# Kernel tuning notes

Measured on AMD Instinct MI355X. Metric: run time of the kernel, lower is better.

## Reference

```python
import jax, jax.numpy as jnp
import numpy as np

N_NODES = 100000
N_EDGES = 1600000
D_FEAT = 64


def setup_inputs() -> dict:
    key = jax.random.key(0)
    k1, k2 = jax.random.split(key)
    x = jax.random.normal(k1, (N_NODES, D_FEAT), dtype=jnp.float32)
    edge_index = jax.random.randint(k2, (2, N_EDGES), 0, N_NODES, dtype=jnp.int64)
    alpha = jnp.ones((), dtype=jnp.float32)
    res_scale = jnp.ones((), dtype=jnp.float32)
    return {"x": x, "alpha": alpha, "res_scale": res_scale, "edge_index": edge_index}


def reference(x, alpha, res_scale, edge_index):
    """LGConv (symmetric gcn_norm, no self-loops) -> alpha-scale -> residual.

    out_i = alpha * sum_{(j->i) in E} x_j / sqrt(deg_i * deg_j) + res_scale * x_i
    """
    n = x.shape[0]
    row, col = edge_index[0], edge_index[1]  # source, target
    # degree from target index (as in PyG gcn_norm with add_self_loops=False)
    deg = jax.ops.segment_sum(jnp.ones(row.shape[0], dtype=x.dtype), col, num_segments=n)
    deg_inv_sqrt = jnp.where(deg > 0, jax.lax.rsqrt(jnp.maximum(deg, 1.0)), 0.0)
    norm = deg_inv_sqrt[row] * deg_inv_sqrt[col]  # (E,)
    msgs = norm[:, None] * x[row]                  # (E, d) gather + scale
    out = jax.ops.segment_sum(msgs, col, num_segments=n)  # scatter-add to targets
    return alpha * out + res_scale * x
```

## Files before the change

### kernel.cpp

```cpp
#include <hip/hip_runtime.h>
#include <hip/hip_bf16.h>

#define D_FEAT 64
#define OVF_CAP 65536
#define EB 4096
#define NBMAX 1024

typedef unsigned int uint32;

__device__ inline float blo(uint32 u) { return __uint_as_float(u << 16); }
__device__ inline float bhi(uint32 u) { return __uint_as_float(u & 0xffff0000u); }
__device__ inline float dinv(int d) { return (d > 0) ? rsqrtf((float)d) : 0.0f; }

__global__ __launch_bounds__(256) void k_hist(const int* __restrict__ col,
                                              int* __restrict__ histT,
                                              const float2* __restrict__ x2,
                                              uint32* __restrict__ xb,
                                              int nhalf, int E, int B, int nb) {
    __shared__ int h[NBMAX];
    for (int i = threadIdx.x; i < nb; i += 256) h[i] = 0;
    __syncthreads();
    const int b = blockIdx.x;
    const int s = b * EB;
    const int e = (s + EB < E) ? s + EB : E;
    for (int i = s + threadIdx.x; i < e; i += 256)
        atomicAdd(&h[col[i] >> 8], 1);
    __syncthreads();
    for (int k = threadIdx.x; k < nb; k += 256)
        histT[(size_t)k * B + b] = h[k];
    const int t = b * 256 + threadIdx.x;
    const int stride = B * 256;
    for (int j = t; j < nhalf; j += stride) {
        float2 v = x2[j];
        __hip_bfloat16 bx = __float2bfloat16(v.x);
        __hip_bfloat16 by = __float2bfloat16(v.y);
        uint32 ux = *reinterpret_cast<unsigned short*>(&bx);
        uint32 uy = *reinterpret_cast<unsigned short*>(&by);
        xb[j] = ux | (uy << 16);
    }
}

__global__ __launch_bounds__(512) void k_colscan(int* __restrict__ histT,
                                                 int* __restrict__ total, int B) {
    __shared__ int sh[512];
    const int k = blockIdx.x;
    int v = (threadIdx.x < B) ? histT[(size_t)k * B + threadIdx.x] : 0;
    sh[threadIdx.x] = v;
    __syncthreads();
    for (int off = 1; off < 512; off <<= 1) {
        int t = (threadIdx.x >= off) ? sh[threadIdx.x - off] : 0;
        __syncthreads();
        sh[threadIdx.x] += t;
        __syncthreads();
    }
    int incl = sh[threadIdx.x];
    if (threadIdx.x < B) histT[(size_t)k * B + threadIdx.x] = incl - v;
    if (threadIdx.x == 511) total[k] = incl;
}

__global__ __launch_bounds__(1024) void k_tinyscan(const int* __restrict__ total,
                                                   int* __restrict__ bstart, int nb) {
    __shared__ int sh[1024];
    int v = (threadIdx.x < nb) ? total[threadIdx.x] : 0;
    sh[threadIdx.x] = v;
    __syncthreads();
    for (int off = 1; off < 1024; off <<= 1) {
        int t = (threadIdx.x >= off) ? sh[threadIdx.x - off] : 0;
        __syncthreads();
        sh[threadIdx.x] += t;
        __syncthreads();
    }
    if (threadIdx.x < nb) bstart[threadIdx.x] = sh[threadIdx.x] - v;
    if (threadIdx.x == nb - 1) bstart[nb] = sh[threadIdx.x];
}

__global__ __launch_bounds__(256) void k_scat3(const int* __restrict__ row,
                                               const int* __restrict__ col,
                                               const int* __restrict__ histT,
                                               const int* __restrict__ bstart,
                                               uint32* __restrict__ binned,
                                               int E, int B, int nb) {
    __shared__ int cur[NBMAX];
    const int b = blockIdx.x;
    for (int k = threadIdx.x; k < nb; k += 256)
        cur[k] = bstart[k] + histT[(size_t)k * B + b];
    __syncthreads();
    const int s = b * EB;
    const int e = (s + EB < E) ? s + EB : E;
    for (int i = s + threadIdx.x; i < e; i += 256) {
        int c = col[i];
        uint32 r = (uint32)row[i];
        int pos = atomicAdd(&cur[c >> 8], 1);
        binned[pos] = (r << 8) | (uint32)(c & 255);
    }
}

__global__ __launch_bounds__(1024) void k_build(const int* __restrict__ bstart,
                                                const uint32* __restrict__ binned,
                                                int* __restrict__ slots,
                                                int* __restrict__ deg,
                                                int2* __restrict__ ovf,
                                                int* __restrict__ ovf_cnt,
                                                int n, int C) {
    __shared__ int cnt[256];
    const int k = blockIdx.x;
    if (threadIdx.x < 256) cnt[threadIdx.x] = 0;
    __syncthreads();
    const int s = bstart[k], e = bstart[k + 1];
    const int base = k << 8;
    for (int i = s + threadIdx.x; i < e; i += 1024) {
        uint32 pk = binned[i];
        int cl = (int)(pk & 255);
        int r  = (int)(pk >> 8);
        int rk = atomicAdd(&cnt[cl], 1);
        int c  = base + cl;
        if (rk < C) {
            slots[(size_t)c * C + rk] = r;
        } else {
            int o = atomicAdd(ovf_cnt, 1);
            if (o < OVF_CAP) ovf[o] = make_int2(r, c);
        }
    }
    __syncthreads();
    int i = base + threadIdx.x;
    if (threadIdx.x < 256 && i < n) deg[i] = cnt[threadIdx.x];
}

__global__ void k_gather4(const uint32* __restrict__ xb,
                          const float4* __restrict__ x4,
                          const int* __restrict__ deg,
                          const int* __restrict__ slots,
                          const float* __restrict__ alpha_p,
                          const float* __restrict__ rs_p,
                          float4* __restrict__ out4, int n, int C) {
    int wid = (blockIdx.x * blockDim.x + threadIdx.x) >> 6;
    if (wid >= n) return;
    const int lane = threadIdx.x & 63;
    const int q = lane >> 4;
    const int l = lane & 15;
    int d = deg[wid];
    int e = (d < C) ? d : C;
    const int* sl = slots + (size_t)wid * C;
    float ax = 0.f, ay = 0.f, az = 0.f, aw = 0.f;
    int k = 0;
    for (; k + 16 <= e; k += 16) {
        int s0 = sl[k + q];
        int s1 = sl[k + 4 + q];
        int s2 = sl[k + 8 + q];
        int s3 = sl[k + 12 + q];
        int d0 = deg[s0], d1 = deg[s1], d2 = deg[s2], d3 = deg[s3];
        uint2 p0 = ((const uint2*)(xb + (size_t)s0 * 32))[l];
        uint2 p1 = ((const uint2*)(xb + (size_t)s1 * 32))[l];
        uint2 p2 = ((const uint2*)(xb + (size_t)s2 * 32))[l];
        uint2 p3 = ((const uint2*)(xb + (size_t)s3 * 32))[l];
        float w0 = dinv(d0), w1 = dinv(d1), w2 = dinv(d2), w3 = dinv(d3);
        ax = fmaf(w0, blo(p0.x), ax); ay = fmaf(w0, bhi(p0.x), ay);
        az = fmaf(w0, blo(p0.y), az); aw = fmaf(w0, bhi(p0.y), aw);
        ax = fmaf(w1, blo(p1.x), ax); ay = fmaf(w1, bhi(p1.x), ay);
        az = fmaf(w1, blo(p1.y), az); aw = fmaf(w1, bhi(p1.y), aw);
        ax = fmaf(w2, blo(p2.x), ax); ay = fmaf(w2, bhi(p2.x), ay);
        az = fmaf(w2, blo(p2.y), az); aw = fmaf(w2, bhi(p2.y), aw);
        ax = fmaf(w3, blo(p3.x), ax); ay = fmaf(w3, bhi(p3.x), ay);
        az = fmaf(w3, blo(p3.y), az); aw = fmaf(w3, bhi(p3.y), aw);
    }
    for (; k < e; k += 4) {
        int kk = k + q;
        if (kk < e) {
            int s0 = sl[kk];
            float w0 = dinv(deg[s0]);
            uint2 p0 = ((const uint2*)(xb + (size_t)s0 * 32))[l];
            ax = fmaf(w0, blo(p0.x), ax); ay = fmaf(w0, bhi(p0.x), ay);
            az = fmaf(w0, blo(p0.y), az); aw = fmaf(w0, bhi(p0.y), aw);
        }
    }
    ax += __shfl_down(ax, 32, 64); ay += __shfl_down(ay, 32, 64);
    az += __shfl_down(az, 32, 64); aw += __shfl_down(aw, 32, 64);
    ax += __shfl_down(ax, 16, 64); ay += __shfl_down(ay, 16, 64);
    az += __shfl_down(az, 16, 64); aw += __shfl_down(aw, 16, 64);
    if (q == 0) {
        float adw = (*alpha_p) * dinv(d);
        float rs  = *rs_p;
        float4 xr = x4[(size_t)wid * 16 + l];
        float4 o;
        o.x = fmaf(adw, ax, rs * xr.x);
        o.y = fmaf(adw, ay, rs * xr.y);
        o.z = fmaf(adw, az, rs * xr.z);
        o.w = fmaf(adw, aw, rs * xr.w);
        out4[(size_t)wid * 16 + l] = o;
    }
}

__global__ void k_ovf(const int2* __restrict__ ovf, const int* __restrict__ cnt_p,
                      const float* __restrict__ x, const int* __restrict__ deg,
                      const float* __restrict__ alpha_p, float* __restrict__ out) {
    int cnt = *cnt_p;
    if (cnt > OVF_CAP) cnt = OVF_CAP;
    if (cnt <= 0) return;
    float a = *alpha_p;
    long long total = (long long)cnt * 64;
    long long stride = (long long)gridDim.x * blockDim.x;
    for (long long idx = blockIdx.x * (long long)blockDim.x + threadIdx.x;
         idx < total; idx += stride) {
        int e = (int)(idx >> 6);
        int f = (int)(idx & 63);
        int2 rc = ovf[e];
        float w = a * dinv(deg[rc.x]) * dinv(deg[rc.y]);
        atomicAdd(&out[(size_t)rc.y * D_FEAT + f], w * x[(size_t)rc.x * D_FEAT + f]);
    }
}

__global__ void k_prep(const float2* __restrict__ x2, uint32* __restrict__ xb,
                       const int* __restrict__ row, const int* __restrict__ col,
                       int* __restrict__ deg, int* __restrict__ slots,
                       int2* __restrict__ ovf, int* __restrict__ ovf_cnt,
                       int nhalf, int E, int C) {
    int t = blockIdx.x * blockDim.x + threadIdx.x;
    if (t < E) {
        int c = col[t];
        int r = row[t];
        int rk = atomicAdd(&deg[c], 1);
        if (rk < C) {
            slots[(size_t)c * C + rk] = r;
        } else {
            int o = atomicAdd(ovf_cnt, 1);
            if (o < OVF_CAP) ovf[o] = make_int2(r, c);
        }
    }
    const int stride = gridDim.x * blockDim.x;
    for (int j = t; j < nhalf; j += stride) {
        float2 v = x2[j];
        __hip_bfloat16 bx = __float2bfloat16(v.x);
        __hip_bfloat16 by = __float2bfloat16(v.y);
        uint32 ux = *reinterpret_cast<unsigned short*>(&bx);
        uint32 uy = *reinterpret_cast<unsigned short*>(&by);
        xb[j] = ux | (uy << 16);
    }
}

static inline char* align_up(char* p, size_t a) {
    return (char*)(((uintptr_t)p + (a - 1)) & ~(uintptr_t)(a - 1));
}

extern "C" void kernel_launch(void* const* d_in, const int* in_sizes, int n_in,
                              void* d_out, int out_size, void* d_ws, size_t ws_size,
                              hipStream_t stream) {
    const float* x         = (const float*)d_in[0];
    const float* alpha     = (const float*)d_in[1];
    const float* res_scale = (const float*)d_in[2];
    const int*   ei        = (const int*)d_in[3];

    const int n = in_sizes[0] / D_FEAT;
    const int E = in_sizes[3] / 2;
    const int* row = ei;
    const int* col = ei + E;

    float* out = (float*)d_out;
    const int nhalf = n * (D_FEAT / 2);
    const int nb = (n + 255) >> 8;
    const int B  = (E + EB - 1) / EB;

    {
        char* p = (char*)d_ws;
        int*    deg     = (int*)p;            p += (size_t)n * 4;
        int*    ovf_cnt = (int*)p;            p += 4;
        int2*   ovf     = (int2*)p;           p += (size_t)OVF_CAP * 8;
        int*    histT   = (int*)p;            p += (size_t)nb * B * 4;
        int*    total   = (int*)p;            p += (size_t)nb * 4;
        int*    bstart  = (int*)p;            p += (size_t)(nb + 1) * 4;
        p = align_up(p, 16);
        uint32* xb      = (uint32*)p;         p += (size_t)n * 128;
        uint32* binned  = (uint32*)p;         p += (size_t)E * 4;
        int*    slots   = (int*)p;
        const size_t fixed = (size_t)(p - (char*)d_ws);

        int C = 0;
        if (ws_size > fixed) {
            size_t c_avail = (ws_size - fixed) / ((size_t)n * 4);
            C = (c_avail > 32) ? 32 : (int)c_avail;
        }
        const bool ok = (C >= 16) && (nb <= NBMAX) && (B <= 512) &&
                        (n <= (NBMAX << 8));
        if (ok) {
            hipMemsetAsync(ovf_cnt, 0, 4, stream);
            k_hist    <<<B, 256, 0, stream>>>(col, histT, (const float2*)x, xb,
                                              nhalf, E, B, nb);
            k_colscan <<<nb, 512, 0, stream>>>(histT, total, B);
            k_tinyscan<<<1, 1024, 0, stream>>>(total, bstart, nb);
            k_scat3   <<<B, 256, 0, stream>>>(row, col, histT, bstart, binned,
                                              E, B, nb);
            k_build   <<<nb, 1024, 0, stream>>>(bstart, binned, slots, deg,
                                                ovf, ovf_cnt, n, C);
            const long long tt = (long long)n * D_FEAT;
            const int blocks = (int)((tt + 255) / 256);
            k_gather4<<<blocks, 256, 0, stream>>>(xb, (const float4*)x, deg, slots,
                                                  alpha, res_scale, (float4*)out,
                                                  n, C);
            k_ovf<<<64, 256, 0, stream>>>(ovf, ovf_cnt, x, deg, alpha, out);
            return;
        }
    }

    {
        char* p = (char*)d_ws;
        int*    deg     = (int*)p;            p += (size_t)n * 4;
        int*    ovf_cnt = (int*)p;            p += 4;
        int2*   ovf     = (int2*)p;           p += (size_t)OVF_CAP * 8;
        p = align_up(p, 16);
        uint32* xb      = (uint32*)p;         p += (size_t)n * 128;
        int*    slots   = (int*)p;
        const size_t fixed = (size_t)(p - (char*)d_ws);
        int C = 0;
        if (ws_size > fixed) {
            size_t c_avail = (ws_size - fixed) / ((size_t)n * 4);
            C = (c_avail > 32) ? 32 : (int)c_avail;
        }
        if (C < 1) return;
        hipMemsetAsync(deg, 0, (size_t)n * 4 + 4, stream);
        k_prep<<<(E + 255) / 256, 256, 0, stream>>>(
            (const float2*)x, xb, row, col, deg, slots, ovf, ovf_cnt,
            nhalf, E, C);
        const long long tt = (long long)n * D_FEAT;
        const int blocks = (int)((tt + 255) / 256);
        k_gather4<<<blocks, 256, 0, stream>>>(xb, (const float4*)x, deg, slots,
                                              alpha, res_scale, (float4*)out, n, C);
        k_ovf<<<64, 256, 0, stream>>>(ovf, ovf_cnt, x, deg, alpha, out);
    }
}
```

Baseline: 188.3 us.

## Prescale bf16 features by source degree and widen gather to 16-byte loads

The bf16 cast of x moves from the histogram kernel into the build kernel, where each node's row is multiplied by its deg^-1/2 before packing. The gather then skips the per-edge deg lookup and rsqrt, and each lane loads a uint4 (8 features) with 8 edges in flight per wave instead of 4. The ovf counter reset moves into the scan kernel, dropping a memset, and the edge block size doubles. The cost is that rounding to bf16 now happens after scaling, and the cast work is tied to the build kernel's per-bin blocks.

```diff
diff --git a/kernel.cpp b/kernel.cpp
--- a/kernel.cpp
+++ b/kernel.cpp
@@ -3,7 +3,7 @@
 
 #define D_FEAT 64
 #define OVF_CAP 65536
-#define EB 4096
+#define EB 8192
 #define NBMAX 1024
 
 typedef unsigned int uint32;
@@ -11,12 +11,17 @@
 __device__ inline float blo(uint32 u) { return __uint_as_float(u << 16); }
 __device__ inline float bhi(uint32 u) { return __uint_as_float(u & 0xffff0000u); }
 __device__ inline float dinv(int d) { return (d > 0) ? rsqrtf((float)d) : 0.0f; }
+__device__ inline uint32 pack_bf16x2(float a, float b) {
+    __hip_bfloat16 ba = __float2bfloat16(a);
+    __hip_bfloat16 bb = __float2bfloat16(b);
+    uint32 ua = *reinterpret_cast<unsigned short*>(&ba);
+    uint32 ub = *reinterpret_cast<unsigned short*>(&bb);
+    return ua | (ub << 16);
+}
 
 __global__ __launch_bounds__(256) void k_hist(const int* __restrict__ col,
                                               int* __restrict__ histT,
-                                              const float2* __restrict__ x2,
-                                              uint32* __restrict__ xb,
-                                              int nhalf, int E, int B, int nb) {
+                                              int E, int B, int nb) {
     __shared__ int h[NBMAX];
     for (int i = threadIdx.x; i < nb; i += 256) h[i] = 0;
     __syncthreads();
@@ -28,16 +33,6 @@
     __syncthreads();
     for (int k = threadIdx.x; k < nb; k += 256)
         histT[(size_t)k * B + b] = h[k];
-    const int t = b * 256 + threadIdx.x;
-    const int stride = B * 256;
-    for (int j = t; j < nhalf; j += stride) {
-        float2 v = x2[j];
-        __hip_bfloat16 bx = __float2bfloat16(v.x);
-        __hip_bfloat16 by = __float2bfloat16(v.y);
-        uint32 ux = *reinterpret_cast<unsigned short*>(&bx);
-        uint32 uy = *reinterpret_cast<unsigned short*>(&by);
-        xb[j] = ux | (uy << 16);
-    }
 }
 
 __global__ __launch_bounds__(512) void k_colscan(int* __restrict__ histT,
@@ -59,7 +54,8 @@
 }
 
 __global__ __launch_bounds__(1024) void k_tinyscan(const int* __restrict__ total,
-                                                   int* __restrict__ bstart, int nb) {
+                                                   int* __restrict__ bstart,
+                                                   int* __restrict__ ovf_cnt, int nb) {
     __shared__ int sh[1024];
     int v = (threadIdx.x < nb) ? total[threadIdx.x] : 0;
     sh[threadIdx.x] = v;
@@ -72,6 +68,7 @@
     }
     if (threadIdx.x < nb) bstart[threadIdx.x] = sh[threadIdx.x] - v;
     if (threadIdx.x == nb - 1) bstart[nb] = sh[threadIdx.x];
+    if (threadIdx.x == 1023) *ovf_cnt = 0;
 }
 
 __global__ __launch_bounds__(256) void k_scat3(const int* __restrict__ row,
@@ -97,12 +94,15 @@
 
 __global__ __launch_bounds__(1024) void k_build(const int* __restrict__ bstart,
                                                 const uint32* __restrict__ binned,
+                                                const float2* __restrict__ x2,
                                                 int* __restrict__ slots,
                                                 int* __restrict__ deg,
+                                                uint32* __restrict__ xb,
                                                 int2* __restrict__ ovf,
                                                 int* __restrict__ ovf_cnt,
                                                 int n, int C) {
     __shared__ int cnt[256];
+    __shared__ float sw[256];
     const int k = blockIdx.x;
     if (threadIdx.x < 256) cnt[threadIdx.x] = 0;
     __syncthreads();
@@ -122,11 +122,24 @@
         }
     }
     __syncthreads();
-    int i = base + threadIdx.x;
-    if (threadIdx.x < 256 && i < n) deg[i] = cnt[threadIdx.x];
-}
-
-__global__ void k_gather4(const uint32* __restrict__ xb,
+    if (threadIdx.x < 256) {
+        int i = base + threadIdx.x;
+        int d = cnt[threadIdx.x];
+        sw[threadIdx.x] = dinv(d);
+        if (i < n) deg[i] = d;
+    }
+    __syncthreads();
+    for (int idx = threadIdx.x; idx < 256 * 32; idx += 1024) {
+        int nl = idx >> 5;
+        int i  = base + nl;
+        if (i >= n) break;
+        float w = sw[nl];
+        float2 v = x2[(size_t)i * 32 + (idx & 31)];
+        xb[(size_t)i * 32 + (idx & 31)] = pack_bf16x2(v.x * w, v.y * w);
+    }
+}
+
+__global__ void k_gather8(const uint32* __restrict__ xb,
                           const float4* __restrict__ x4,
                           const int* __restrict__ deg,
                           const int* __restrict__ slots,
@@ -136,57 +149,57 @@
     int wid = (blockIdx.x * blockDim.x + threadIdx.x) >> 6;
     if (wid >= n) return;
     const int lane = threadIdx.x & 63;
-    const int q = lane >> 4;
-    const int l = lane & 15;
+    const int q = lane >> 3;
+    const int l = lane & 7;
     int d = deg[wid];
     int e = (d < C) ? d : C;
     const int* sl = slots + (size_t)wid * C;
-    float ax = 0.f, ay = 0.f, az = 0.f, aw = 0.f;
+    float a0 = 0.f, a1 = 0.f, a2 = 0.f, a3 = 0.f;
+    float a4 = 0.f, a5 = 0.f, a6 = 0.f, a7 = 0.f;
     int k = 0;
     for (; k + 16 <= e; k += 16) {
         int s0 = sl[k + q];
-        int s1 = sl[k + 4 + q];
-        int s2 = sl[k + 8 + q];
-        int s3 = sl[k + 12 + q];
-        int d0 = deg[s0], d1 = deg[s1], d2 = deg[s2], d3 = deg[s3];
-        uint2 p0 = ((const uint2*)(xb + (size_t)s0 * 32))[l];
-        uint2 p1 = ((const uint2*)(xb + (size_t)s1 * 32))[l];
-        uint2 p2 = ((const uint2*)(xb + (size_t)s2 * 32))[l];
-        uint2 p3 = ((const uint2*)(xb + (size_t)s3 * 32))[l];
-        float w0 = dinv(d0), w1 = dinv(d1), w2 = dinv(d2), w3 = dinv(d3);
-        ax = fmaf(w0, blo(p0.x), ax); ay = fmaf(w0, bhi(p0.x), ay);
-        az = fmaf(w0, blo(p0.y), az); aw = fmaf(w0, bhi(p0.y), aw);
-        ax = fmaf(w1, blo(p1.x), ax); ay = fmaf(w1, bhi(p1.x), ay);
-        az = fmaf(w1, blo(p1.y), az); aw = fmaf(w1, bhi(p1.y), aw);
-        ax = fmaf(w2, blo(p2.x), ax); ay = fmaf(w2, bhi(p2.x), ay);
-        az = fmaf(w2, blo(p2.y), az); aw = fmaf(w2, bhi(p2.y), aw);
-        ax = fmaf(w3, blo(p3.x), ax); ay = fmaf(w3, bhi(p3.x), ay);
-        az = fmaf(w3, blo(p3.y), az); aw = fmaf(w3, bhi(p3.y), aw);
-    }
-    for (; k < e; k += 4) {
+        int s1 = sl[k + 8 + q];
+        uint4 p0 = ((const uint4*)(xb + (size_t)s0 * 32))[l];
+        uint4 p1 = ((const uint4*)(xb + (size_t)s1 * 32))[l];
+        a0 += blo(p0.x); a1 += bhi(p0.x); a2 += blo(p0.y); a3 += bhi(p0.y);
+        a4 += blo(p0.z); a5 += bhi(p0.z); a6 += blo(p0.w); a7 += bhi(p0.w);
+        a0 += blo(p1.x); a1 += bhi(p1.x); a2 += blo(p1.y); a3 += bhi(p1.y);
+        a4 += blo(p1.z); a5 += bhi(p1.z); a6 += blo(p1.w); a7 += bhi(p1.w);
+    }
+    for (; k < e; k += 8) {
         int kk = k + q;
         if (kk < e) {
             int s0 = sl[kk];
-            float w0 = dinv(deg[s0]);
-            uint2 p0 = ((const uint2*)(xb + (size_t)s0 * 32))[l];
-            ax = fmaf(w0, blo(p0.x), ax); ay = fmaf(w0, bhi(p0.x), ay);
-            az = fmaf(w0, blo(p0.y), az); aw = fmaf(w0, bhi(p0.y), aw);
-        }
-    }
-    ax += __shfl_down(ax, 32, 64); ay += __shfl_down(ay, 32, 64);
-    az += __shfl_down(az, 32, 64); aw += __shfl_down(aw, 32, 64);
-    ax += __shfl_down(ax, 16, 64); ay += __shfl_down(ay, 16, 64);
-    az += __shfl_down(az, 16, 64); aw += __shfl_down(aw, 16, 64);
+            uint4 p0 = ((const uint4*)(xb + (size_t)s0 * 32))[l];
+            a0 += blo(p0.x); a1 += bhi(p0.x); a2 += blo(p0.y); a3 += bhi(p0.y);
+            a4 += blo(p0.z); a5 += bhi(p0.z); a6 += blo(p0.w); a7 += bhi(p0.w);
+        }
+    }
+    #pragma unroll
+    for (int off = 32; off >= 8; off >>= 1) {
+        a0 += __shfl_down(a0, off, 64); a1 += __shfl_down(a1, off, 64);
+        a2 += __shfl_down(a2, off, 64); a3 += __shfl_down(a3, off, 64);
+        a4 += __shfl_down(a4, off, 64); a5 += __shfl_down(a5, off, 64);
+        a6 += __shfl_down(a6, off, 64); a7 += __shfl_down(a7, off, 64);
+    }
     if (q == 0) {
         float adw = (*alpha_p) * dinv(d);
         float rs  = *rs_p;
-        float4 xr = x4[(size_t)wid * 16 + l];
-        float4 o;
-        o.x = fmaf(adw, ax, rs * xr.x);
-        o.y = fmaf(adw, ay, rs * xr.y);
-        o.z = fmaf(adw, az, rs * xr.z);
-        o.w = fmaf(adw, aw, rs * xr.w);
-        out4[(size_t)wid * 16 + l] = o;
+        size_t base = (size_t)wid * 16 + 2 * l;
+        float4 xr0 = x4[base];
+        float4 xr1 = x4[base + 1];
+        float4 o0, o1;
+        o0.x = fmaf(adw, a0, rs * xr0.x);
+        o0.y = fmaf(adw, a1, rs * xr0.y);
+        o0.z = fmaf(adw, a2, rs * xr0.z);
+        o0.w = fmaf(adw, a3, rs * xr0.w);
+        o1.x = fmaf(adw, a4, rs * xr1.x);
+        o1.y = fmaf(adw, a5, rs * xr1.y);
+        o1.z = fmaf(adw, a6, rs * xr1.z);
+        o1.w = fmaf(adw, a7, rs * xr1.w);
+        out4[base]     = o0;
+        out4[base + 1] = o1;
     }
 }
 
@@ -209,11 +222,10 @@
     }
 }
 
-__global__ void k_prep(const float2* __restrict__ x2, uint32* __restrict__ xb,
-                       const int* __restrict__ row, const int* __restrict__ col,
+__global__ void k_prep(const int* __restrict__ row, const int* __restrict__ col,
                        int* __restrict__ deg, int* __restrict__ slots,
                        int2* __restrict__ ovf, int* __restrict__ ovf_cnt,
-                       int nhalf, int E, int C) {
+                       int E, int C) {
     int t = blockIdx.x * blockDim.x + threadIdx.x;
     if (t < E) {
         int c = col[t];
@@ -226,14 +238,14 @@
             if (o < OVF_CAP) ovf[o] = make_int2(r, c);
         }
     }
-    const int stride = gridDim.x * blockDim.x;
-    for (int j = t; j < nhalf; j += stride) {
-        float2 v = x2[j];
-        __hip_bfloat16 bx = __float2bfloat16(v.x);
-        __hip_bfloat16 by = __float2bfloat16(v.y);
-        uint32 ux = *reinterpret_cast<unsigned short*>(&bx);
-        uint32 uy = *reinterpret_cast<unsigned short*>(&by);
-        xb[j] = ux | (uy << 16);
+}
+__global__ void k_cast(const float2* __restrict__ x2, const int* __restrict__ deg,
+                       uint32* __restrict__ xb, int nhalf) {
+    int t = blockIdx.x * blockDim.x + threadIdx.x;
+    if (t < nhalf) {
+        float w = dinv(deg[t >> 5]);
+        float2 v = x2[t];
+        xb[t] = pack_bf16x2(v.x * w, v.y * w);
     }
 }
 
@@ -281,18 +293,16 @@
         const bool ok = (C >= 16) && (nb <= NBMAX) && (B <= 512) &&
                         (n <= (NBMAX << 8));
         if (ok) {
-            hipMemsetAsync(ovf_cnt, 0, 4, stream);
-            k_hist    <<<B, 256, 0, stream>>>(col, histT, (const float2*)x, xb,
-                                              nhalf, E, B, nb);
+            k_hist    <<<B, 256, 0, stream>>>(col, histT, E, B, nb);
             k_colscan <<<nb, 512, 0, stream>>>(histT, total, B);
-            k_tinyscan<<<1, 1024, 0, stream>>>(total, bstart, nb);
+            k_tinyscan<<<1, 1024, 0, stream>>>(total, bstart, ovf_cnt, nb);
             k_scat3   <<<B, 256, 0, stream>>>(row, col, histT, bstart, binned,
                                               E, B, nb);
-            k_build   <<<nb, 1024, 0, stream>>>(bstart, binned, slots, deg,
-                                                ovf, ovf_cnt, n, C);
+            k_build   <<<nb, 1024, 0, stream>>>(bstart, binned, (const float2*)x,
+                                                slots, deg, xb, ovf, ovf_cnt, n, C);
             const long long tt = (long long)n * D_FEAT;
             const int blocks = (int)((tt + 255) / 256);
-            k_gather4<<<blocks, 256, 0, stream>>>(xb, (const float4*)x, deg, slots,
+            k_gather8<<<blocks, 256, 0, stream>>>(xb, (const float4*)x, deg, slots,
                                                   alpha, res_scale, (float4*)out,
                                                   n, C);
             k_ovf<<<64, 256, 0, stream>>>(ovf, ovf_cnt, x, deg, alpha, out);
@@ -316,12 +326,13 @@
         }
         if (C < 1) return;
         hipMemsetAsync(deg, 0, (size_t)n * 4 + 4, stream);
-        k_prep<<<(E + 255) / 256, 256, 0, stream>>>(
-            (const float2*)x, xb, row, col, deg, slots, ovf, ovf_cnt,
-            nhalf, E, C);
+        k_prep<<<(E + 255) / 256, 256, 0, stream>>>(row, col, deg, slots,
+                                                    ovf, ovf_cnt, E, C);
+        k_cast<<<(nhalf + 255) / 256, 256, 0, stream>>>((const float2*)x, deg,
+                                                        xb, nhalf);
         const long long tt = (long long)n * D_FEAT;
         const int blocks = (int)((tt + 255) / 256);
-        k_gather4<<<blocks, 256, 0, stream>>>(xb, (const float4*)x, deg, slots,
+        k_gather8<<<blocks, 256, 0, stream>>>(xb, (const float4*)x, deg, slots,
                                               alpha, res_scale, (float4*)out, n, C);
         k_ovf<<<64, 256, 0, stream>>>(ovf, ovf_cnt, x, deg, alpha, out);
     }
```

Measured after the change: 188.8 us. No clear change (+0.2%).
